# Optimization experiments

Hardware: AMD Instinct MI355X
Metric: run time of the kernel (lower is better)

The kernel has to match this reference:

```python
import jax, jax.numpy as jnp
import numpy as np
from math import sqrt

B, C, L = 32, 32, 512            # batch, channels(enc_in), seq_len
INTRA, INTER = 1024, 256          # memory-bank intra_len, inter_len
DCP, DDE = 64, 512                # compress width (retrieved set size), denoise hidden
SCALE = 0.05


def setup_inputs() -> dict:
    key = jax.random.key(0)
    ks = jax.random.split(key, 12)
    s = 0.02  # small init scale for weights
    return {
        "x_loc": jax.random.normal(ks[0], (B, C, L), jnp.float32),
        "indices": jax.random.randint(ks[1], (B, L), 0, INTRA),
        "map_raw": jax.random.normal(ks[2], (C, INTRA, INTER), jnp.float32),
        # compress: Linear(INTER->DCP), ReLU, Linear(DCP->DCP)
        "cW1": jax.random.normal(ks[3], (DCP, INTER), jnp.float32) * s,
        "cb1": jnp.zeros((DCP,), jnp.float32),
        "cW2": jax.random.normal(ks[4], (DCP, DCP), jnp.float32) * s,
        "cb2": jnp.zeros((DCP,), jnp.float32),
        # denoise: Linear(INTRA->DDE), ReLU, Linear(DDE->INTRA)
        "dW1": jax.random.normal(ks[5], (DDE, INTRA), jnp.float32) * s,
        "db1": jnp.zeros((DDE,), jnp.float32),
        "dW2": jax.random.normal(ks[6], (INTRA, DDE), jnp.float32) * s,
        "db2": jnp.zeros((INTRA,), jnp.float32),
        "lamda1": jnp.zeros((C, 1), jnp.float32),
        "lamda2": jnp.zeros((1, L), jnp.float32),
    }


def reference(x_loc, indices, map_raw, cW1, cb1, cW2, cb2,
              dW1, db1, dW2, db2, lamda1, lamda2):
    # compress along inter_len: (C, INTRA, INTER) -> (C, INTRA, DCP)
    map_tmp = jax.nn.relu(map_raw @ cW1.T + cb1) @ cW2.T + cb2
    map_tmp = jnp.swapaxes(map_tmp, 1, 2)            # (C, DCP, INTRA)
    # denoise along intra_len
    map_st = jax.nn.relu(map_tmp @ dW1.T + db1) @ dW2.T + db2  # (C, DCP, INTRA)
    # gather: map_dy[b,c,d,l] = map_st[c, d, indices[b,l]]
    map_dy = jnp.transpose(map_st[:, :, indices], (2, 0, 1, 3))  # (B, C, DCP, L)
    # l1 similarity (negative L1 distance, scaled by sqrt(L))
    scores = -jnp.sum(jnp.abs(x_loc[:, :, None, :] - map_dy), axis=-1) / sqrt(L)  # (B,C,DCP)
    scores = jax.nn.softmax(scores * SCALE, axis=2)
    lamda = jax.nn.sigmoid(lamda1) @ jax.nn.sigmoid(lamda2)     # (C, L)
    x_global = jnp.einsum('bchl,bch->bcl', map_dy, scores)      # (B, C, L)
    return x_global * lamda + x_loc * (1.0 - lamda)
```

## Files before the change

### kernel.cpp

```cpp
#include <hip/hip_runtime.h>
#include <hip/hip_bf16.h>

#define Bn 32
#define Cn 32
#define Ln 512
#define INTRA 1024
#define INTER 256
#define DCP 64
#define DDE 512
#define SCALEF 0.05f

typedef __attribute__((ext_vector_type(8))) short short8;
typedef __attribute__((ext_vector_type(4))) float floatx4;

__device__ __forceinline__ short bf16_of(float f) {
    union { float f; unsigned u; } v; v.f = f;
    unsigned r = (v.u + 0x7FFFu + ((v.u >> 16) & 1u)) >> 16;
    return (short)r;
}
__device__ __forceinline__ float f_of_bf16(short h) {
    union { unsigned u; float f; } v;
    v.u = ((unsigned)(unsigned short)h) << 16;
    return v.f;
}
__device__ __forceinline__ short8 cvt8(float4 a, float4 b) {
    short8 r;
    r[0] = bf16_of(a.x); r[1] = bf16_of(a.y); r[2] = bf16_of(a.z); r[3] = bf16_of(a.w);
    r[4] = bf16_of(b.x); r[5] = bf16_of(b.y); r[6] = bf16_of(b.z); r[7] = bf16_of(b.w);
    return r;
}

__global__ __launch_bounds__(256) void compress_fused(
    const float* __restrict__ map_raw, const float* __restrict__ cW1,
    const float* __restrict__ cb1, const float* __restrict__ cW2,
    const float* __restrict__ cb2, short* __restrict__ M1T)
{
    const int c  = blockIdx.y;
    const int m0 = blockIdx.x * 64;
    const float* A = map_raw + ((long)c * INTRA + m0) * INTER;

    __shared__ short Asb[64 * 72];
    __shared__ short Bsb[64 * 72];
    __shared__ short Tsb[64 * 72];

    const int t = threadIdx.x, w = t >> 6, lane = t & 63;
    const int ln = lane & 15, quad = lane >> 4;
    const int sr = t >> 2, sk = (t & 3) * 16;

    const float* ap = A + sr * INTER + sk;
    const float* bp = cW1 + sr * INTER + sk;

    floatx4 acc[4] = {};
    float4 a0 = *(const float4*)(ap),     a1 = *(const float4*)(ap + 4);
    float4 a2 = *(const float4*)(ap + 8), a3 = *(const float4*)(ap + 12);
    float4 b0 = *(const float4*)(bp),     b1 = *(const float4*)(bp + 4);
    float4 b2 = *(const float4*)(bp + 8), b3 = *(const float4*)(bp + 12);

    for (int k0 = 0; k0 < INTER; k0 += 64) {
        __syncthreads();
        *(short8*)&Asb[sr * 72 + sk]     = cvt8(a0, a1);
        *(short8*)&Asb[sr * 72 + sk + 8] = cvt8(a2, a3);
        *(short8*)&Bsb[sr * 72 + sk]     = cvt8(b0, b1);
        *(short8*)&Bsb[sr * 72 + sk + 8] = cvt8(b2, b3);
        __syncthreads();
        const int kn = k0 + 64;
        if (kn < INTER) {
            a0 = *(const float4*)(ap + kn);     a1 = *(const float4*)(ap + kn + 4);
            a2 = *(const float4*)(ap + kn + 8); a3 = *(const float4*)(ap + kn + 12);
            b0 = *(const float4*)(bp + kn);     b1 = *(const float4*)(bp + kn + 4);
            b2 = *(const float4*)(bp + kn + 8); b3 = *(const float4*)(bp + kn + 12);
        }
        #pragma unroll
        for (int kc = 0; kc < 2; ++kc) {
            short8 af = *(const short8*)&Asb[(w * 16 + ln) * 72 + kc * 32 + quad * 8];
            #pragma unroll
            for (int nt = 0; nt < 4; ++nt) {
                short8 bf = *(const short8*)&Bsb[(nt * 16 + ln) * 72 + kc * 32 + quad * 8];
                acc[nt] = __builtin_amdgcn_mfma_f32_16x16x32_bf16(af, bf, acc[nt], 0, 0, 0);
            }
        }
    }
    __syncthreads();

    #pragma unroll
    for (int nt = 0; nt < 4; ++nt) {
        const int n = nt * 16 + ln;
        const float b = cb1[n];
        #pragma unroll
        for (int r = 0; r < 4; ++r)
            Tsb[(w * 16 + quad * 4 + r) * 72 + n] = bf16_of(fmaxf(acc[nt][r] + b, 0.f));
    }
    __syncthreads();

    floatx4 acc2[4] = {};
    #pragma unroll
    for (int ks = 0; ks < 2; ++ks) {
        short8 af = *(const short8*)&Tsb[(w * 16 + ln) * 72 + ks * 32 + quad * 8];
        #pragma unroll
        for (int nt = 0; nt < 4; ++nt) {
            const float* wp = cW2 + (nt * 16 + ln) * 64 + ks * 32 + quad * 8;
            short8 bf = cvt8(*(const float4*)wp, *(const float4*)(wp + 4));
            acc2[nt] = __builtin_amdgcn_mfma_f32_16x16x32_bf16(af, bf, acc2[nt], 0, 0, 0);
        }
    }

    short* outp = M1T + (long)c * 64 * INTRA;
    #pragma unroll
    for (int nt = 0; nt < 4; ++nt) {
        const int n = nt * 16 + ln;
        const float b = cb2[n];
        short t0 = bf16_of(acc2[nt][0] + b);
        short t1 = bf16_of(acc2[nt][1] + b);
        short t2 = bf16_of(acc2[nt][2] + b);
        short t3 = bf16_of(acc2[nt][3] + b);
        *(short4*)(outp + (long)n * INTRA + m0 + w * 16 + quad * 4) =
            make_short4(t0, t1, t2, t3);
    }
}

__global__ __launch_bounds__(256) void gemm_dn1(
    const float* __restrict__ dW1, const short* __restrict__ M1T,
    const float* __restrict__ db1, short* __restrict__ HT)
{
    const int c  = blockIdx.y;
    const int h0 = blockIdx.x * 32;

    __shared__ short Asb[32 * 136];
    __shared__ short Bsb[64 * 136];

    const int t = threadIdx.x, w = t >> 6, lane = t & 63;
    const int ln = lane & 15, quad = lane >> 4;
    const int ar = t >> 3, ak = (t & 7) * 16;
    const int br = t >> 2, bk = (t & 3) * 32;

    const float* Ap = dW1 + (long)(h0 + ar) * INTRA + ak;
    const short* Bp = M1T + (long)c * 64 * INTRA + (long)br * INTRA + bk;

    floatx4 acc[2] = {};
    float4 fa0 = *(const float4*)(Ap),     fa1 = *(const float4*)(Ap + 4);
    float4 fa2 = *(const float4*)(Ap + 8), fa3 = *(const float4*)(Ap + 12);
    short8 sb0 = *(const short8*)(Bp),      sb1 = *(const short8*)(Bp + 8);
    short8 sb2 = *(const short8*)(Bp + 16), sb3 = *(const short8*)(Bp + 24);

    const int mb = (w & 1) * 16;
    const int nb = (w >> 1) * 2;

    for (int k0 = 0; k0 < INTRA; k0 += 128) {
        __syncthreads();
        *(short8*)&Asb[ar * 136 + ak]      = cvt8(fa0, fa1);
        *(short8*)&Asb[ar * 136 + ak + 8]  = cvt8(fa2, fa3);
        *(short8*)&Bsb[br * 136 + bk]      = sb0;
        *(short8*)&Bsb[br * 136 + bk + 8]  = sb1;
        *(short8*)&Bsb[br * 136 + bk + 16] = sb2;
        *(short8*)&Bsb[br * 136 + bk + 24] = sb3;
        __syncthreads();
        const int kn = k0 + 128;
        if (kn < INTRA) {
            fa0 = *(const float4*)(Ap + kn);     fa1 = *(const float4*)(Ap + kn + 4);
            fa2 = *(const float4*)(Ap + kn + 8); fa3 = *(const float4*)(Ap + kn + 12);
            sb0 = *(const short8*)(Bp + kn);      sb1 = *(const short8*)(Bp + kn + 8);
            sb2 = *(const short8*)(Bp + kn + 16); sb3 = *(const short8*)(Bp + kn + 24);
        }
        #pragma unroll
        for (int kc = 0; kc < 4; ++kc) {
            short8 af  = *(const short8*)&Asb[(mb + ln) * 136 + kc * 32 + quad * 8];
            short8 bf0 = *(const short8*)&Bsb[((nb + 0) * 16 + ln) * 136 + kc * 32 + quad * 8];
            short8 bf1 = *(const short8*)&Bsb[((nb + 1) * 16 + ln) * 136 + kc * 32 + quad * 8];
            acc[0] = __builtin_amdgcn_mfma_f32_16x16x32_bf16(af, bf0, acc[0], 0, 0, 0);
            acc[1] = __builtin_amdgcn_mfma_f32_16x16x32_bf16(af, bf1, acc[1], 0, 0, 0);
        }
    }

    float bm[4];
    #pragma unroll
    for (int r = 0; r < 4; ++r) bm[r] = db1[h0 + mb + quad * 4 + r];

    short* outp = HT + (long)c * 64 * DDE;
    #pragma unroll
    for (int j = 0; j < 2; ++j) {
        const int d = (nb + j) * 16 + ln;
        float v0 = fmaxf(acc[j][0] + bm[0], 0.f);
        float v1 = fmaxf(acc[j][1] + bm[1], 0.f);
        float v2 = fmaxf(acc[j][2] + bm[2], 0.f);
        float v3 = fmaxf(acc[j][3] + bm[3], 0.f);
        *(short4*)(outp + (long)d * DDE + h0 + mb + quad * 4) =
            make_short4(bf16_of(v0), bf16_of(v1), bf16_of(v2), bf16_of(v3));
    }
}

__global__ __launch_bounds__(256) void gemm_dn2(
    const short* __restrict__ HT, const float* __restrict__ dW2,
    const float* __restrict__ db2, short* __restrict__ S16)
{
    const int c  = blockIdx.y;
    const int n0 = blockIdx.x * 64;

    __shared__ short Asb[64 * 136];
    __shared__ short Bsb[64 * 136];

    const int t = threadIdx.x, w = t >> 6, lane = t & 63;
    const int ln = lane & 15, quad = lane >> 4;
    const int ar = t >> 2, ak = (t & 3) * 32;

    const short* Ap = HT + (long)c * 64 * DDE + (long)ar * DDE + ak;
    const float* Bp = dW2 + (long)(n0 + ar) * DDE + ak;

    floatx4 acc[4] = {};
    short8 sa0 = *(const short8*)(Ap),      sa1 = *(const short8*)(Ap + 8);
    short8 sa2 = *(const short8*)(Ap + 16), sa3 = *(const short8*)(Ap + 24);
    float4 fb0 = *(const float4*)(Bp),      fb1 = *(const float4*)(Bp + 4);
    float4 fb2 = *(const float4*)(Bp + 8),  fb3 = *(const float4*)(Bp + 12);
    float4 fb4 = *(const float4*)(Bp + 16), fb5 = *(const float4*)(Bp + 20);
    float4 fb6 = *(const float4*)(Bp + 24), fb7 = *(const float4*)(Bp + 28);

    for (int k0 = 0; k0 < DDE; k0 += 128) {
        __syncthreads();
        *(short8*)&Asb[ar * 136 + ak]      = sa0;
        *(short8*)&Asb[ar * 136 + ak + 8]  = sa1;
        *(short8*)&Asb[ar * 136 + ak + 16] = sa2;
        *(short8*)&Asb[ar * 136 + ak + 24] = sa3;
        *(short8*)&Bsb[ar * 136 + ak]      = cvt8(fb0, fb1);
        *(short8*)&Bsb[ar * 136 + ak + 8]  = cvt8(fb2, fb3);
        *(short8*)&Bsb[ar * 136 + ak + 16] = cvt8(fb4, fb5);
        *(short8*)&Bsb[ar * 136 + ak + 24] = cvt8(fb6, fb7);
        __syncthreads();
        const int kn = k0 + 128;
        if (kn < DDE) {
            sa0 = *(const short8*)(Ap + kn);      sa1 = *(const short8*)(Ap + kn + 8);
            sa2 = *(const short8*)(Ap + kn + 16); sa3 = *(const short8*)(Ap + kn + 24);
            fb0 = *(const float4*)(Bp + kn);      fb1 = *(const float4*)(Bp + kn + 4);
            fb2 = *(const float4*)(Bp + kn + 8);  fb3 = *(const float4*)(Bp + kn + 12);
            fb4 = *(const float4*)(Bp + kn + 16); fb5 = *(const float4*)(Bp + kn + 20);
            fb6 = *(const float4*)(Bp + kn + 24); fb7 = *(const float4*)(Bp + kn + 28);
        }
        #pragma unroll
        for (int kc = 0; kc < 4; ++kc) {
            short8 af = *(const short8*)&Asb[(w * 16 + ln) * 136 + kc * 32 + quad * 8];
            #pragma unroll
            for (int nt = 0; nt < 4; ++nt) {
                short8 bf = *(const short8*)&Bsb[(nt * 16 + ln) * 136 + kc * 32 + quad * 8];
                acc[nt] = __builtin_amdgcn_mfma_f32_16x16x32_bf16(af, bf, acc[nt], 0, 0, 0);
            }
        }
    }

    const int d0 = w * 16 + quad * 4;
    #pragma unroll
    for (int nt = 0; nt < 4; ++nt) {
        const int i = n0 + nt * 16 + ln;
        const float bb = db2[i];
        short t0 = bf16_of(acc[nt][0] + bb);
        short t1 = bf16_of(acc[nt][1] + bb);
        short t2 = bf16_of(acc[nt][2] + bb);
        short t3 = bf16_of(acc[nt][3] + bb);
        *(short4*)(S16 + ((long)c * INTRA + i) * DCP + d0) = make_short4(t0, t1, t2, t3);
    }
}

__global__ __launch_bounds__(256) void fuse_kernel(
    const float* __restrict__ x_loc, const int* __restrict__ indices,
    const short* __restrict__ S16, const float* __restrict__ lamda1,
    const float* __restrict__ lamda2, float* __restrict__ out)
{
    const int c = blockIdx.x;
    const int b = blockIdx.y;

    __shared__ float xs[Ln];
    __shared__ int   idx[Ln];
    __shared__ float red[4][DCP];
    __shared__ short wbf[DCP];
    __shared__ float ob[Ln];

    const int t = threadIdx.x;
    const float* xp = x_loc + ((long)b * Cn + c) * Ln;
    const int*   ip = indices + (long)b * Ln;
    ((float2*)xs)[t] = ((const float2*)xp)[t];
    ((int2*)idx)[t]  = ((const int2*)ip)[t];
    __syncthreads();

    const short* Sc = S16 + (long)c * INTRA * DCP;
    const int lane = t & 63;
    const int w    = t >> 6;
    const int r    = lane >> 4;
    const int dg   = lane & 15;

    float s0 = 0.f, s1 = 0.f, s2 = 0.f, s3 = 0.f;
    #pragma unroll 4
    for (int i = 0; i < 32; ++i) {
        const int lbase = w * 128 + i * 4;
        const int row   = idx[lbase + r];
        short4 g = *(const short4*)(Sc + (long)row * DCP + dg * 4);
        const float x = xs[lbase + r];
        s0 += fabsf(x - f_of_bf16(g.x));
        s1 += fabsf(x - f_of_bf16(g.y));
        s2 += fabsf(x - f_of_bf16(g.z));
        s3 += fabsf(x - f_of_bf16(g.w));
    }
    s0 += __shfl_xor(s0, 16); s0 += __shfl_xor(s0, 32);
    s1 += __shfl_xor(s1, 16); s1 += __shfl_xor(s1, 32);
    s2 += __shfl_xor(s2, 16); s2 += __shfl_xor(s2, 32);
    s3 += __shfl_xor(s3, 16); s3 += __shfl_xor(s3, 32);
    if (lane < 16) {
        red[w][dg * 4 + 0] = s0;
        red[w][dg * 4 + 1] = s1;
        red[w][dg * 4 + 2] = s2;
        red[w][dg * 4 + 3] = s3;
    }
    __syncthreads();

    if (t < DCP) {
        float sc = red[0][t] + red[1][t] + red[2][t] + red[3][t];
        sc = -sc * (SCALEF * 0.044194173824159216f);
        float m = sc;
        #pragma unroll
        for (int o = 32; o > 0; o >>= 1) m = fmaxf(m, __shfl_xor(m, o));
        float e = __expf(sc - m);
        float ssum = e;
        #pragma unroll
        for (int o = 32; o > 0; o >>= 1) ssum += __shfl_xor(ssum, o);
        wbf[t] = bf16_of(e / ssum);
    }
    __syncthreads();

    const int quad = lane >> 4;
    const int ln16 = lane & 15;
    short8 bw0 = *(const short8*)&wbf[quad * 8];
    short8 bw1 = *(const short8*)&wbf[32 + quad * 8];

    #pragma unroll
    for (int mt = 0; mt < 8; ++mt) {
        const int mrow = w * 128 + mt * 16 + ln16;
        const short* rp = Sc + (long)idx[mrow] * DCP;
        short8 a0 = *(const short8*)(rp + quad * 8);
        short8 a1 = *(const short8*)(rp + 32 + quad * 8);
        floatx4 acc = {};
        acc = __builtin_amdgcn_mfma_f32_16x16x32_bf16(a0, bw0, acc, 0, 0, 0);
        acc = __builtin_amdgcn_mfma_f32_16x16x32_bf16(a1, bw1, acc, 0, 0, 0);
        if (ln16 == 0) {
            const int l0 = w * 128 + mt * 16 + quad * 4;
            ob[l0 + 0] = acc[0];
            ob[l0 + 1] = acc[1];
            ob[l0 + 2] = acc[2];
            ob[l0 + 3] = acc[3];
        }
    }
    __syncthreads();

    const float lam1 = 1.f / (1.f + __expf(-lamda1[c]));
    #pragma unroll
    for (int j = 0; j < 2; ++j) {
        const int l = t + j * 256;
        const float lam = lam1 * (1.f / (1.f + __expf(-lamda2[l])));
        out[((long)b * Cn + c) * Ln + l] = ob[l] * lam + xs[l] * (1.f - lam);
    }
}

extern "C" void kernel_launch(void* const* d_in, const int* in_sizes, int n_in,
                              void* d_out, int out_size, void* d_ws, size_t ws_size,
                              hipStream_t stream)
{
    const float* x_loc   = (const float*)d_in[0];
    const int*   indices = (const int*)d_in[1];
    const float* map_raw = (const float*)d_in[2];
    const float* cW1     = (const float*)d_in[3];
    const float* cb1     = (const float*)d_in[4];
    const float* cW2     = (const float*)d_in[5];
    const float* cb2     = (const float*)d_in[6];
    const float* dW1     = (const float*)d_in[7];
    const float* db1     = (const float*)d_in[8];
    const float* dW2     = (const float*)d_in[9];
    const float* db2     = (const float*)d_in[10];
    const float* lamda1  = (const float*)d_in[11];
    const float* lamda2  = (const float*)d_in[12];
    float* out = (float*)d_out;

    short* wsS = (short*)d_ws;
    short* M1T = wsS;
    short* HT  = M1T + 2097152;
    short* S16 = HT + 1048576;

    compress_fused<<<dim3(INTRA / 64, Cn), 256, 0, stream>>>(
        map_raw, cW1, cb1, cW2, cb2, M1T);

    gemm_dn1<<<dim3(DDE / 32, Cn), 256, 0, stream>>>(
        dW1, M1T, db1, HT);

    gemm_dn2<<<dim3(INTRA / 64, Cn), 256, 0, stream>>>(
        HT, dW2, db2, S16);

    fuse_kernel<<<dim3(Cn, Bn), 256, 0, stream>>>(
        x_loc, indices, S16, lamda1, lamda2, out);
}
```

Measured before the change: 144.8 us.

## Merge four kernels into one cooperative persistent kernel with grid syncs

Replaces four separate kernel launches (compress, denoise layer 1, denoise layer 2, gather/softmax fuse) with a single cooperative kernel of 512 blocks. Stages are separated by grid.sync and thread fences, and shared memory is reused across phases. The goal is to remove per-launch overhead and inter-kernel gaps. The trade-offs are the cost of grid-wide barriers, a fixed grid size that limits parallelism in the last stage (two (b,c) pairs per block), and the occupancy constraint that all blocks must be co-resident.

```diff
diff --git a/kernel.cpp b/kernel.cpp
--- a/kernel.cpp
+++ b/kernel.cpp
@@ -1,5 +1,8 @@
 #include <hip/hip_runtime.h>
 #include <hip/hip_bf16.h>
+#include <hip/hip_cooperative_groups.h>
+
+namespace cg = cooperative_groups;
 
 #define Bn 32
 #define Cn 32
@@ -30,328 +33,340 @@
     return r;
 }
 
-__global__ __launch_bounds__(256) void compress_fused(
-    const float* __restrict__ map_raw, const float* __restrict__ cW1,
-    const float* __restrict__ cb1, const float* __restrict__ cW2,
-    const float* __restrict__ cb2, short* __restrict__ M1T)
+__global__ __launch_bounds__(256, 2) void mega(
+    const float* __restrict__ x_loc, const int* __restrict__ indices,
+    const float* __restrict__ map_raw,
+    const float* __restrict__ cW1, const float* __restrict__ cb1,
+    const float* __restrict__ cW2, const float* __restrict__ cb2,
+    const float* __restrict__ dW1, const float* __restrict__ db1,
+    const float* __restrict__ dW2, const float* __restrict__ db2,
+    const float* __restrict__ lamda1, const float* __restrict__ lamda2,
+    short* __restrict__ M1T, short* __restrict__ HT, short* __restrict__ S16,
+    float* __restrict__ out)
 {
-    const int c  = blockIdx.y;
-    const int m0 = blockIdx.x * 64;
-    const float* A = map_raw + ((long)c * INTRA + m0) * INTER;
-
-    __shared__ short Asb[64 * 72];
-    __shared__ short Bsb[64 * 72];
-    __shared__ short Tsb[64 * 72];
-
-    const int t = threadIdx.x, w = t >> 6, lane = t & 63;
-    const int ln = lane & 15, quad = lane >> 4;
-    const int sr = t >> 2, sk = (t & 3) * 16;
-
-    const float* ap = A + sr * INTER + sk;
-    const float* bp = cW1 + sr * INTER + sk;
-
-    floatx4 acc[4] = {};
-    float4 a0 = *(const float4*)(ap),     a1 = *(const float4*)(ap + 4);
-    float4 a2 = *(const float4*)(ap + 8), a3 = *(const float4*)(ap + 12);
-    float4 b0 = *(const float4*)(bp),     b1 = *(const float4*)(bp + 4);
-    float4 b2 = *(const float4*)(bp + 8), b3 = *(const float4*)(bp + 12);
-
-    for (int k0 = 0; k0 < INTER; k0 += 64) {
+    cg::grid_group grid = cg::this_grid();
+
+    __shared__ __align__(16) short smem[17408];
+
+    const int bid  = blockIdx.x;
+    const int t    = threadIdx.x;
+    const int w    = t >> 6;
+    const int lane = t & 63;
+    const int ln   = lane & 15;
+    const int quad = lane >> 4;
+
+    {
+        const int c  = bid >> 4;
+        const int m0 = (bid & 15) * 64;
+        const float* A = map_raw + ((long)c * INTRA + m0) * INTER;
+
+        short* Asb = smem;
+        short* Bsb = smem + 4608;
+        short* Tsb = smem + 9216;
+
+        const int sr = t >> 2, sk = (t & 3) * 16;
+        const float* ap = A + sr * INTER + sk;
+        const float* bp = cW1 + sr * INTER + sk;
+
+        floatx4 acc[4] = {};
+        float4 a0 = *(const float4*)(ap),     a1 = *(const float4*)(ap + 4);
+        float4 a2 = *(const float4*)(ap + 8), a3 = *(const float4*)(ap + 12);
+        float4 b0 = *(const float4*)(bp),     b1 = *(const float4*)(bp + 4);
+        float4 b2 = *(const float4*)(bp + 8), b3 = *(const float4*)(bp + 12);
+
+        for (int k0 = 0; k0 < INTER; k0 += 64) {
+            __syncthreads();
+            *(short8*)&Asb[sr * 72 + sk]     = cvt8(a0, a1);
+            *(short8*)&Asb[sr * 72 + sk + 8] = cvt8(a2, a3);
+            *(short8*)&Bsb[sr * 72 + sk]     = cvt8(b0, b1);
+            *(short8*)&Bsb[sr * 72 + sk + 8] = cvt8(b2, b3);
+            __syncthreads();
+            const int kn = k0 + 64;
+            if (kn < INTER) {
+                a0 = *(const float4*)(ap + kn);     a1 = *(const float4*)(ap + kn + 4);
+                a2 = *(const float4*)(ap + kn + 8); a3 = *(const float4*)(ap + kn + 12);
+                b0 = *(const float4*)(bp + kn);     b1 = *(const float4*)(bp + kn + 4);
+                b2 = *(const float4*)(bp + kn + 8); b3 = *(const float4*)(bp + kn + 12);
+            }
+            #pragma unroll
+            for (int kc = 0; kc < 2; ++kc) {
+                short8 af = *(const short8*)&Asb[(w * 16 + ln) * 72 + kc * 32 + quad * 8];
+                #pragma unroll
+                for (int nt = 0; nt < 4; ++nt) {
+                    short8 bf = *(const short8*)&Bsb[(nt * 16 + ln) * 72 + kc * 32 + quad * 8];
+                    acc[nt] = __builtin_amdgcn_mfma_f32_16x16x32_bf16(af, bf, acc[nt], 0, 0, 0);
+                }
+            }
+        }
         __syncthreads();
-        *(short8*)&Asb[sr * 72 + sk]     = cvt8(a0, a1);
-        *(short8*)&Asb[sr * 72 + sk + 8] = cvt8(a2, a3);
-        *(short8*)&Bsb[sr * 72 + sk]     = cvt8(b0, b1);
-        *(short8*)&Bsb[sr * 72 + sk + 8] = cvt8(b2, b3);
+
+        #pragma unroll
+        for (int nt = 0; nt < 4; ++nt) {
+            const int n = nt * 16 + ln;
+            const float b = cb1[n];
+            #pragma unroll
+            for (int r = 0; r < 4; ++r)
+                Tsb[(w * 16 + quad * 4 + r) * 72 + n] = bf16_of(fmaxf(acc[nt][r] + b, 0.f));
+        }
         __syncthreads();
-        const int kn = k0 + 64;
-        if (kn < INTER) {
-            a0 = *(const float4*)(ap + kn);     a1 = *(const float4*)(ap + kn + 4);
-            a2 = *(const float4*)(ap + kn + 8); a3 = *(const float4*)(ap + kn + 12);
-            b0 = *(const float4*)(bp + kn);     b1 = *(const float4*)(bp + kn + 4);
-            b2 = *(const float4*)(bp + kn + 8); b3 = *(const float4*)(bp + kn + 12);
-        }
-        #pragma unroll
-        for (int kc = 0; kc < 2; ++kc) {
-            short8 af = *(const short8*)&Asb[(w * 16 + ln) * 72 + kc * 32 + quad * 8];
+
+        floatx4 acc2[4] = {};
+        #pragma unroll
+        for (int ks = 0; ks < 2; ++ks) {
+            short8 af = *(const short8*)&Tsb[(w * 16 + ln) * 72 + ks * 32 + quad * 8];
             #pragma unroll
             for (int nt = 0; nt < 4; ++nt) {
-                short8 bf = *(const short8*)&Bsb[(nt * 16 + ln) * 72 + kc * 32 + quad * 8];
-                acc[nt] = __builtin_amdgcn_mfma_f32_16x16x32_bf16(af, bf, acc[nt], 0, 0, 0);
-            }
+                const float* wp = cW2 + (nt * 16 + ln) * 64 + ks * 32 + quad * 8;
+                short8 bf = cvt8(*(const float4*)wp, *(const float4*)(wp + 4));
+                acc2[nt] = __builtin_amdgcn_mfma_f32_16x16x32_bf16(af, bf, acc2[nt], 0, 0, 0);
+            }
+        }
+
+        short* outp = M1T + (long)c * 64 * INTRA;
+        #pragma unroll
+        for (int nt = 0; nt < 4; ++nt) {
+            const int n = nt * 16 + ln;
+            const float b = cb2[n];
+            short t0 = bf16_of(acc2[nt][0] + b);
+            short t1 = bf16_of(acc2[nt][1] + b);
+            short t2 = bf16_of(acc2[nt][2] + b);
+            short t3 = bf16_of(acc2[nt][3] + b);
+            *(short4*)(outp + (long)n * INTRA + m0 + w * 16 + quad * 4) =
+                make_short4(t0, t1, t2, t3);
         }
     }
-    __syncthreads();
-
-    #pragma unroll
-    for (int nt = 0; nt < 4; ++nt) {
-        const int n = nt * 16 + ln;
-        const float b = cb1[n];
-        #pragma unroll
-        for (int r = 0; r < 4; ++r)
-            Tsb[(w * 16 + quad * 4 + r) * 72 + n] = bf16_of(fmaxf(acc[nt][r] + b, 0.f));
+
+    __threadfence();
+    grid.sync();
+
+    {
+        const int c  = bid >> 4;
+        const int h0 = (bid & 15) * 32;
+
+        short* Asb = smem;
+        short* Bsb = smem + 4352;
+
+        const int ar = t >> 3, ak = (t & 7) * 16;
+        const int br = t >> 2, bk = (t & 3) * 32;
+
+        const float* Ap = dW1 + (long)(h0 + ar) * INTRA + ak;
+        const short* Bp = M1T + (long)c * 64 * INTRA + (long)br * INTRA + bk;
+
+        floatx4 acc[2] = {};
+        float4 fa0 = *(const float4*)(Ap),     fa1 = *(const float4*)(Ap + 4);
+        float4 fa2 = *(const float4*)(Ap + 8), fa3 = *(const float4*)(Ap + 12);
+        short8 sb0 = *(const short8*)(Bp),      sb1 = *(const short8*)(Bp + 8);
+        short8 sb2 = *(const short8*)(Bp + 16), sb3 = *(const short8*)(Bp + 24);
+
+        const int mb = (w & 1) * 16;
+        const int nb = (w >> 1) * 2;
+
+        for (int k0 = 0; k0 < INTRA; k0 += 128) {
+            __syncthreads();
+            *(short8*)&Asb[ar * 136 + ak]      = cvt8(fa0, fa1);
+            *(short8*)&Asb[ar * 136 + ak + 8]  = cvt8(fa2, fa3);
+            *(short8*)&Bsb[br * 136 + bk]      = sb0;
+            *(short8*)&Bsb[br * 136 + bk + 8]  = sb1;
+            *(short8*)&Bsb[br * 136 + bk + 16] = sb2;
+            *(short8*)&Bsb[br * 136 + bk + 24] = sb3;
+            __syncthreads();
+            const int kn = k0 + 128;
+            if (kn < INTRA) {
+                fa0 = *(const float4*)(Ap + kn);     fa1 = *(const float4*)(Ap + kn + 4);
+                fa2 = *(const float4*)(Ap + kn + 8); fa3 = *(const float4*)(Ap + kn + 12);
+                sb0 = *(const short8*)(Bp + kn);      sb1 = *(const short8*)(Bp + kn + 8);
+                sb2 = *(const short8*)(Bp + kn + 16); sb3 = *(const short8*)(Bp + kn + 24);
+            }
+            #pragma unroll
+            for (int kc = 0; kc < 4; ++kc) {
+                short8 af  = *(const short8*)&Asb[(mb + ln) * 136 + kc * 32 + quad * 8];
+                short8 bf0 = *(const short8*)&Bsb[((nb + 0) * 16 + ln) * 136 + kc * 32 + quad * 8];
+                short8 bf1 = *(const short8*)&Bsb[((nb + 1) * 16 + ln) * 136 + kc * 32 + quad * 8];
+                acc[0] = __builtin_amdgcn_mfma_f32_16x16x32_bf16(af, bf0, acc[0], 0, 0, 0);
+                acc[1] = __builtin_amdgcn_mfma_f32_16x16x32_bf16(af, bf1, acc[1], 0, 0, 0);
+            }
+        }
+
+        float bm[4];
+        #pragma unroll
+        for (int r = 0; r < 4; ++r) bm[r] = db1[h0 + mb + quad * 4 + r];
+
+        short* outp = HT + (long)c * 64 * DDE;
+        #pragma unroll
+        for (int j = 0; j < 2; ++j) {
+            const int d = (nb + j) * 16 + ln;
+            float v0 = fmaxf(acc[j][0] + bm[0], 0.f);
+            float v1 = fmaxf(acc[j][1] + bm[1], 0.f);
+            float v2 = fmaxf(acc[j][2] + bm[2], 0.f);
+            float v3 = fmaxf(acc[j][3] + bm[3], 0.f);
+            *(short4*)(outp + (long)d * DDE + h0 + mb + quad * 4) =
+                make_short4(bf16_of(v0), bf16_of(v1), bf16_of(v2), bf16_of(v3));
+        }
     }
-    __syncthreads();
-
-    floatx4 acc2[4] = {};
-    #pragma unroll
-    for (int ks = 0; ks < 2; ++ks) {
-        short8 af = *(const short8*)&Tsb[(w * 16 + ln) * 72 + ks * 32 + quad * 8];
+
+    __threadfence();
+    grid.sync();
+
+    {
+        const int c  = bid >> 4;
+        const int n0 = (bid & 15) * 64;
+
+        short* Asb = smem;
+        short* Bsb = smem + 8704;
+
+        const int ar = t >> 2, ak = (t & 3) * 32;
+
+        const short* Ap = HT + (long)c * 64 * DDE + (long)ar * DDE + ak;
+        const float* Bp = dW2 + (long)(n0 + ar) * DDE + ak;
+
+        floatx4 acc[4] = {};
+        short8 sa0 = *(const short8*)(Ap),      sa1 = *(const short8*)(Ap + 8);
+        short8 sa2 = *(const short8*)(Ap + 16), sa3 = *(const short8*)(Ap + 24);
+        float4 fb0 = *(const float4*)(Bp),      fb1 = *(const float4*)(Bp + 4);
+        float4 fb2 = *(const float4*)(Bp + 8),  fb3 = *(const float4*)(Bp + 12);
+        float4 fb4 = *(const float4*)(Bp + 16), fb5 = *(const float4*)(Bp + 20);
+        float4 fb6 = *(const float4*)(Bp + 24), fb7 = *(const float4*)(Bp + 28);
+
+        for (int k0 = 0; k0 < DDE; k0 += 128) {
+            __syncthreads();
+            *(short8*)&Asb[ar * 136 + ak]      = sa0;
+            *(short8*)&Asb[ar * 136 + ak + 8]  = sa1;
+            *(short8*)&Asb[ar * 136 + ak + 16] = sa2;
+            *(short8*)&Asb[ar * 136 + ak + 24] = sa3;
+            *(short8*)&Bsb[ar * 136 + ak]      = cvt8(fb0, fb1);
+            *(short8*)&Bsb[ar * 136 + ak + 8]  = cvt8(fb2, fb3);
+            *(short8*)&Bsb[ar * 136 + ak + 16] = cvt8(fb4, fb5);
+            *(short8*)&Bsb[ar * 136 + ak + 24] = cvt8(fb6, fb7);
+            __syncthreads();
+            const int kn = k0 + 128;
+            if (kn < DDE) {
+                sa0 = *(const short8*)(Ap + kn);      sa1 = *(const short8*)(Ap + kn + 8);
+                sa2 = *(const short8*)(Ap + kn + 16); sa3 = *(const short8*)(Ap + kn + 24);
+                fb0 = *(const float4*)(Bp + kn);      fb1 = *(const float4*)(Bp + kn + 4);
+                fb2 = *(const float4*)(Bp + kn + 8);  fb3 = *(const float4*)(Bp + kn + 12);
+                fb4 = *(const float4*)(Bp + kn + 16); fb5 = *(const float4*)(Bp + kn + 20);
+                fb6 = *(const float4*)(Bp + kn + 24); fb7 = *(const float4*)(Bp + kn + 28);
+            }
+            #pragma unroll
+            for (int kc = 0; kc < 4; ++kc) {
+                short8 af = *(const short8*)&Asb[(w * 16 + ln) * 136 + kc * 32 + quad * 8];
+                #pragma unroll
+                for (int nt = 0; nt < 4; ++nt) {
+                    short8 bf = *(const short8*)&Bsb[(nt * 16 + ln) * 136 + kc * 32 + quad * 8];
+                    acc[nt] = __builtin_amdgcn_mfma_f32_16x16x32_bf16(af, bf, acc[nt], 0, 0, 0);
+                }
+            }
+        }
+
+        const int d0 = w * 16 + quad * 4;
         #pragma unroll
         for (int nt = 0; nt < 4; ++nt) {
-            const float* wp = cW2 + (nt * 16 + ln) * 64 + ks * 32 + quad * 8;
-            short8 bf = cvt8(*(const float4*)wp, *(const float4*)(wp + 4));
-            acc2[nt] = __builtin_amdgcn_mfma_f32_16x16x32_bf16(af, bf, acc2[nt], 0, 0, 0);
+            const int i = n0 + nt * 16 + ln;
+            const float bb = db2[i];
+            short t0 = bf16_of(acc[nt][0] + bb);
+            short t1 = bf16_of(acc[nt][1] + bb);
+            short t2 = bf16_of(acc[nt][2] + bb);
+            short t3 = bf16_of(acc[nt][3] + bb);
+            *(short4*)(S16 + ((long)c * INTRA + i) * DCP + d0) = make_short4(t0, t1, t2, t3);
         }
     }
 
-    short* outp = M1T + (long)c * 64 * INTRA;
-    #pragma unroll
-    for (int nt = 0; nt < 4; ++nt) {
-        const int n = nt * 16 + ln;
-        const float b = cb2[n];
-        short t0 = bf16_of(acc2[nt][0] + b);
-        short t1 = bf16_of(acc2[nt][1] + b);
-        short t2 = bf16_of(acc2[nt][2] + b);
-        short t3 = bf16_of(acc2[nt][3] + b);
-        *(short4*)(outp + (long)n * INTRA + m0 + w * 16 + quad * 4) =
-            make_short4(t0, t1, t2, t3);
-    }
-}
-
-__global__ __launch_bounds__(256) void gemm_dn1(
-    const float* __restrict__ dW1, const short* __restrict__ M1T,
-    const float* __restrict__ db1, short* __restrict__ HT)
-{
-    const int c  = blockIdx.y;
-    const int h0 = blockIdx.x * 32;
-
-    __shared__ short Asb[32 * 136];
-    __shared__ short Bsb[64 * 136];
-
-    const int t = threadIdx.x, w = t >> 6, lane = t & 63;
-    const int ln = lane & 15, quad = lane >> 4;
-    const int ar = t >> 3, ak = (t & 7) * 16;
-    const int br = t >> 2, bk = (t & 3) * 32;
-
-    const float* Ap = dW1 + (long)(h0 + ar) * INTRA + ak;
-    const short* Bp = M1T + (long)c * 64 * INTRA + (long)br * INTRA + bk;
-
-    floatx4 acc[2] = {};
-    float4 fa0 = *(const float4*)(Ap),     fa1 = *(const float4*)(Ap + 4);
-    float4 fa2 = *(const float4*)(Ap + 8), fa3 = *(const float4*)(Ap + 12);
-    short8 sb0 = *(const short8*)(Bp),      sb1 = *(const short8*)(Bp + 8);
-    short8 sb2 = *(const short8*)(Bp + 16), sb3 = *(const short8*)(Bp + 24);
-
-    const int mb = (w & 1) * 16;
-    const int nb = (w >> 1) * 2;
-
-    for (int k0 = 0; k0 < INTRA; k0 += 128) {
-        __syncthreads();
-        *(short8*)&Asb[ar * 136 + ak]      = cvt8(fa0, fa1);
-        *(short8*)&Asb[ar * 136 + ak + 8]  = cvt8(fa2, fa3);
-        *(short8*)&Bsb[br * 136 + bk]      = sb0;
-        *(short8*)&Bsb[br * 136 + bk + 8]  = sb1;
-        *(short8*)&Bsb[br * 136 + bk + 16] = sb2;
-        *(short8*)&Bsb[br * 136 + bk + 24] = sb3;
-        __syncthreads();
-        const int kn = k0 + 128;
-        if (kn < INTRA) {
-            fa0 = *(const float4*)(Ap + kn);     fa1 = *(const float4*)(Ap + kn + 4);
-            fa2 = *(const float4*)(Ap + kn + 8); fa3 = *(const float4*)(Ap + kn + 12);
-            sb0 = *(const short8*)(Bp + kn);      sb1 = *(const short8*)(Bp + kn + 8);
-            sb2 = *(const short8*)(Bp + kn + 16); sb3 = *(const short8*)(Bp + kn + 24);
-        }
-        #pragma unroll
-        for (int kc = 0; kc < 4; ++kc) {
-            short8 af  = *(const short8*)&Asb[(mb + ln) * 136 + kc * 32 + quad * 8];
-            short8 bf0 = *(const short8*)&Bsb[((nb + 0) * 16 + ln) * 136 + kc * 32 + quad * 8];
-            short8 bf1 = *(const short8*)&Bsb[((nb + 1) * 16 + ln) * 136 + kc * 32 + quad * 8];
-            acc[0] = __builtin_amdgcn_mfma_f32_16x16x32_bf16(af, bf0, acc[0], 0, 0, 0);
-            acc[1] = __builtin_amdgcn_mfma_f32_16x16x32_bf16(af, bf1, acc[1], 0, 0, 0);
-        }
-    }
-
-    float bm[4];
-    #pragma unroll
-    for (int r = 0; r < 4; ++r) bm[r] = db1[h0 + mb + quad * 4 + r];
-
-    short* outp = HT + (long)c * 64 * DDE;
-    #pragma unroll
-    for (int j = 0; j < 2; ++j) {
-        const int d = (nb + j) * 16 + ln;
-        float v0 = fmaxf(acc[j][0] + bm[0], 0.f);
-        float v1 = fmaxf(acc[j][1] + bm[1], 0.f);
-        float v2 = fmaxf(acc[j][2] + bm[2], 0.f);
-        float v3 = fmaxf(acc[j][3] + bm[3], 0.f);
-        *(short4*)(outp + (long)d * DDE + h0 + mb + quad * 4) =
-            make_short4(bf16_of(v0), bf16_of(v1), bf16_of(v2), bf16_of(v3));
-    }
-}
-
-__global__ __launch_bounds__(256) void gemm_dn2(
-    const short* __restrict__ HT, const float* __restrict__ dW2,
-    const float* __restrict__ db2, short* __restrict__ S16)
-{
-    const int c  = blockIdx.y;
-    const int n0 = blockIdx.x * 64;
-
-    __shared__ short Asb[64 * 136];
-    __shared__ short Bsb[64 * 136];
-
-    const int t = threadIdx.x, w = t >> 6, lane = t & 63;
-    const int ln = lane & 15, quad = lane >> 4;
-    const int ar = t >> 2, ak = (t & 3) * 32;
-
-    const short* Ap = HT + (long)c * 64 * DDE + (long)ar * DDE + ak;
-    const float* Bp = dW2 + (long)(n0 + ar) * DDE + ak;
-
-    floatx4 acc[4] = {};
-    short8 sa0 = *(const short8*)(Ap),      sa1 = *(const short8*)(Ap + 8);
-    short8 sa2 = *(const short8*)(Ap + 16), sa3 = *(const short8*)(Ap + 24);
-    float4 fb0 = *(const float4*)(Bp),      fb1 = *(const float4*)(Bp + 4);
-    float4 fb2 = *(const float4*)(Bp + 8),  fb3 = *(const float4*)(Bp + 12);
-    float4 fb4 = *(const float4*)(Bp + 16), fb5 = *(const float4*)(Bp + 20);
-    float4 fb6 = *(const float4*)(Bp + 24), fb7 = *(const float4*)(Bp + 28);
-
-    for (int k0 = 0; k0 < DDE; k0 += 128) {
-        __syncthreads();
-        *(short8*)&Asb[ar * 136 + ak]      = sa0;
-        *(short8*)&Asb[ar * 136 + ak + 8]  = sa1;
-        *(short8*)&Asb[ar * 136 + ak + 16] = sa2;
-        *(short8*)&Asb[ar * 136 + ak + 24] = sa3;
-        *(short8*)&Bsb[ar * 136 + ak]      = cvt8(fb0, fb1);
-        *(short8*)&Bsb[ar * 136 + ak + 8]  = cvt8(fb2, fb3);
-        *(short8*)&Bsb[ar * 136 + ak + 16] = cvt8(fb4, fb5);
-        *(short8*)&Bsb[ar * 136 + ak + 24] = cvt8(fb6, fb7);
-        __syncthreads();
-        const int kn = k0 + 128;
-        if (kn < DDE) {
-            sa0 = *(const short8*)(Ap + kn);      sa1 = *(const short8*)(Ap + kn + 8);
-            sa2 = *(const short8*)(Ap + kn + 16); sa3 = *(const short8*)(Ap + kn + 24);
-            fb0 = *(const float4*)(Bp + kn);      fb1 = *(const float4*)(Bp + kn + 4);
-            fb2 = *(const float4*)(Bp + kn + 8);  fb3 = *(const float4*)(Bp + kn + 12);
-            fb4 = *(const float4*)(Bp + kn + 16); fb5 = *(const float4*)(Bp + kn + 20);
-            fb6 = *(const float4*)(Bp + kn + 24); fb7 = *(const float4*)(Bp + kn + 28);
-        }
-        #pragma unroll
-        for (int kc = 0; kc < 4; ++kc) {
-            short8 af = *(const short8*)&Asb[(w * 16 + ln) * 136 + kc * 32 + quad * 8];
-            #pragma unroll
-            for (int nt = 0; nt < 4; ++nt) {
-                short8 bf = *(const short8*)&Bsb[(nt * 16 + ln) * 136 + kc * 32 + quad * 8];
-                acc[nt] = __builtin_amdgcn_mfma_f32_16x16x32_bf16(af, bf, acc[nt], 0, 0, 0);
-            }
-        }
-    }
-
-    const int d0 = w * 16 + quad * 4;
-    #pragma unroll
-    for (int nt = 0; nt < 4; ++nt) {
-        const int i = n0 + nt * 16 + ln;
-        const float bb = db2[i];
-        short t0 = bf16_of(acc[nt][0] + bb);
-        short t1 = bf16_of(acc[nt][1] + bb);
-        short t2 = bf16_of(acc[nt][2] + bb);
-        short t3 = bf16_of(acc[nt][3] + bb);
-        *(short4*)(S16 + ((long)c * INTRA + i) * DCP + d0) = make_short4(t0, t1, t2, t3);
-    }
-}
-
-__global__ __launch_bounds__(256) void fuse_kernel(
-    const float* __restrict__ x_loc, const int* __restrict__ indices,
-    const short* __restrict__ S16, const float* __restrict__ lamda1,
-    const float* __restrict__ lamda2, float* __restrict__ out)
-{
-    const int c = blockIdx.x;
-    const int b = blockIdx.y;
-
-    __shared__ float xs[Ln];
-    __shared__ int   idx[Ln];
-    __shared__ float red[4][DCP];
-    __shared__ short wbf[DCP];
-    __shared__ float ob[Ln];
-
-    const int t = threadIdx.x;
-    const float* xp = x_loc + ((long)b * Cn + c) * Ln;
-    const int*   ip = indices + (long)b * Ln;
-    ((float2*)xs)[t] = ((const float2*)xp)[t];
-    ((int2*)idx)[t]  = ((const int2*)ip)[t];
-    __syncthreads();
-
-    const short* Sc = S16 + (long)c * INTRA * DCP;
-    const int lane = t & 63;
-    const int w    = t >> 6;
-    const int r    = lane >> 4;
-    const int dg   = lane & 15;
-
-    float s0 = 0.f, s1 = 0.f, s2 = 0.f, s3 = 0.f;
-    #pragma unroll 4
-    for (int i = 0; i < 32; ++i) {
-        const int lbase = w * 128 + i * 4;
-        const int row   = idx[lbase + r];
-        short4 g = *(const short4*)(Sc + (long)row * DCP + dg * 4);
-        const float x = xs[lbase + r];
-        s0 += fabsf(x - f_of_bf16(g.x));
-        s1 += fabsf(x - f_of_bf16(g.y));
-        s2 += fabsf(x - f_of_bf16(g.z));
-        s3 += fabsf(x - f_of_bf16(g.w));
-    }
-    s0 += __shfl_xor(s0, 16); s0 += __shfl_xor(s0, 32);
-    s1 += __shfl_xor(s1, 16); s1 += __shfl_xor(s1, 32);
-    s2 += __shfl_xor(s2, 16); s2 += __shfl_xor(s2, 32);
-    s3 += __shfl_xor(s3, 16); s3 += __shfl_xor(s3, 32);
-    if (lane < 16) {
-        red[w][dg * 4 + 0] = s0;
-        red[w][dg * 4 + 1] = s1;
-        red[w][dg * 4 + 2] = s2;
-        red[w][dg * 4 + 3] = s3;
-    }
-    __syncthreads();
-
-    if (t < DCP) {
-        float sc = red[0][t] + red[1][t] + red[2][t] + red[3][t];
-        sc = -sc * (SCALEF * 0.044194173824159216f);
-        float m = sc;
-        #pragma unroll
-        for (int o = 32; o > 0; o >>= 1) m = fmaxf(m, __shfl_xor(m, o));
-        float e = __expf(sc - m);
-        float ssum = e;
-        #pragma unroll
-        for (int o = 32; o > 0; o >>= 1) ssum += __shfl_xor(ssum, o);
-        wbf[t] = bf16_of(e / ssum);
-    }
-    __syncthreads();
-
-    const int quad = lane >> 4;
-    const int ln16 = lane & 15;
-    short8 bw0 = *(const short8*)&wbf[quad * 8];
-    short8 bw1 = *(const short8*)&wbf[32 + quad * 8];
-
-    #pragma unroll
-    for (int mt = 0; mt < 8; ++mt) {
-        const int mrow = w * 128 + mt * 16 + ln16;
-        const short* rp = Sc + (long)idx[mrow] * DCP;
-        short8 a0 = *(const short8*)(rp + quad * 8);
-        short8 a1 = *(const short8*)(rp + 32 + quad * 8);
-        floatx4 acc = {};
-        acc = __builtin_amdgcn_mfma_f32_16x16x32_bf16(a0, bw0, acc, 0, 0, 0);
-        acc = __builtin_amdgcn_mfma_f32_16x16x32_bf16(a1, bw1, acc, 0, 0, 0);
-        if (ln16 == 0) {
-            const int l0 = w * 128 + mt * 16 + quad * 4;
-            ob[l0 + 0] = acc[0];
-            ob[l0 + 1] = acc[1];
-            ob[l0 + 2] = acc[2];
-            ob[l0 + 3] = acc[3];
-        }
-    }
-    __syncthreads();
-
-    const float lam1 = 1.f / (1.f + __expf(-lamda1[c]));
-    #pragma unroll
-    for (int j = 0; j < 2; ++j) {
-        const int l = t + j * 256;
-        const float lam = lam1 * (1.f / (1.f + __expf(-lamda2[l])));
-        out[((long)b * Cn + c) * Ln + l] = ob[l] * lam + xs[l] * (1.f - lam);
+    __threadfence();
+    grid.sync();
+
+    {
+        float* xs  = (float*)smem;
+        int*   idx = (int*)(smem + 1024);
+        float (*red)[DCP] = (float(*)[DCP])(smem + 2048);
+        short* wbf = smem + 2560;
+        float* ob  = (float*)(smem + 2624);
+
+        const int r  = lane >> 4;
+        const int dg = lane & 15;
+
+        #pragma unroll
+        for (int pp = 0; pp < 2; ++pp) {
+            const int p = bid + pp * 512;
+            const int c = p & 31;
+            const int b = p >> 5;
+
+            const float* xp = x_loc + ((long)b * Cn + c) * Ln;
+            const int*   ip = indices + (long)b * Ln;
+            ((float2*)xs)[t] = ((const float2*)xp)[t];
+            ((int2*)idx)[t]  = ((const int2*)ip)[t];
+            __syncthreads();
+
+            const short* Sc = S16 + (long)c * INTRA * DCP;
+
+            float s0 = 0.f, s1 = 0.f, s2 = 0.f, s3 = 0.f;
+            #pragma unroll 4
+            for (int i = 0; i < 32; ++i) {
+                const int lbase = w * 128 + i * 4;
+                const int row   = idx[lbase + r];
+                short4 g = *(const short4*)(Sc + (long)row * DCP + dg * 4);
+                const float x = xs[lbase + r];
+                s0 += fabsf(x - f_of_bf16(g.x));
+                s1 += fabsf(x - f_of_bf16(g.y));
+                s2 += fabsf(x - f_of_bf16(g.z));
+                s3 += fabsf(x - f_of_bf16(g.w));
+            }
+            s0 += __shfl_xor(s0, 16); s0 += __shfl_xor(s0, 32);
+            s1 += __shfl_xor(s1, 16); s1 += __shfl_xor(s1, 32);
+            s2 += __shfl_xor(s2, 16); s2 += __shfl_xor(s2, 32);
+            s3 += __shfl_xor(s3, 16); s3 += __shfl_xor(s3, 32);
+            if (lane < 16) {
+                red[w][dg * 4 + 0] = s0;
+                red[w][dg * 4 + 1] = s1;
+                red[w][dg * 4 + 2] = s2;
+                red[w][dg * 4 + 3] = s3;
+            }
+            __syncthreads();
+
+            if (t < DCP) {
+                float sc = red[0][t] + red[1][t] + red[2][t] + red[3][t];
+                sc = -sc * (SCALEF * 0.044194173824159216f);
+                float m = sc;
+                #pragma unroll
+                for (int o = 32; o > 0; o >>= 1) m = fmaxf(m, __shfl_xor(m, o));
+                float e = __expf(sc - m);
+                float ssum = e;
+                #pragma unroll
+                for (int o = 32; o > 0; o >>= 1) ssum += __shfl_xor(ssum, o);
+                wbf[t] = bf16_of(e / ssum);
+            }
+            __syncthreads();
+
+            short8 bw0 = *(const short8*)&wbf[quad * 8];
+            short8 bw1 = *(const short8*)&wbf[32 + quad * 8];
+
+            #pragma unroll
+            for (int mt = 0; mt < 8; ++mt) {
+                const int mrow = w * 128 + mt * 16 + ln;
+                const short* rp = Sc + (long)idx[mrow] * DCP;
+                short8 a0 = *(const short8*)(rp + quad * 8);
+                short8 a1 = *(const short8*)(rp + 32 + quad * 8);
+                floatx4 acc = {};
+                acc = __builtin_amdgcn_mfma_f32_16x16x32_bf16(a0, bw0, acc, 0, 0, 0);
+                acc = __builtin_amdgcn_mfma_f32_16x16x32_bf16(a1, bw1, acc, 0, 0, 0);
+                if (ln == 0) {
+                    const int l0 = w * 128 + mt * 16 + quad * 4;
+                    ob[l0 + 0] = acc[0];
+                    ob[l0 + 1] = acc[1];
+                    ob[l0 + 2] = acc[2];
+                    ob[l0 + 3] = acc[3];
+                }
+            }
+            __syncthreads();
+
+            const float lam1 = 1.f / (1.f + __expf(-lamda1[c]));
+            #pragma unroll
+            for (int j = 0; j < 2; ++j) {
+                const int l = t + j * 256;
+                const float lam = lam1 * (1.f / (1.f + __expf(-lamda2[l])));
+                out[((long)b * Cn + c) * Ln + l] = ob[l] * lam + xs[l] * (1.f - lam);
+            }
+            __syncthreads();
+        }
     }
 }
 
@@ -379,15 +394,14 @@
     short* HT  = M1T + 2097152;
     short* S16 = HT + 1048576;
 
-    compress_fused<<<dim3(INTRA / 64, Cn), 256, 0, stream>>>(
-        map_raw, cW1, cb1, cW2, cb2, M1T);
-
-    gemm_dn1<<<dim3(DDE / 32, Cn), 256, 0, stream>>>(
-        dW1, M1T, db1, HT);
-
-    gemm_dn2<<<dim3(INTRA / 64, Cn), 256, 0, stream>>>(
-        HT, dW2, db2, S16);
-
-    fuse_kernel<<<dim3(Cn, Bn), 256, 0, stream>>>(
-        x_loc, indices, S16, lamda1, lamda2, out);
+    void* args[] = {
+        (void*)&x_loc, (void*)&indices, (void*)&map_raw,
+        (void*)&cW1, (void*)&cb1, (void*)&cW2, (void*)&cb2,
+        (void*)&dW1, (void*)&db1, (void*)&dW2, (void*)&db2,
+        (void*)&lamda1, (void*)&lamda2,
+        (void*)&M1T, (void*)&HT, (void*)&S16, (void*)&out
+    };
+
+    hipLaunchCooperativeKernel((void*)mega, dim3(512), dim3(256),
+                               args, 0, stream);
 }
```

Result: slower. 462.3 us (+219.3%).
